# Performance work log

Measured on AMD Instinct MI355X. Metric: run time of the kernel, lower is better.

## Reference

```python
import jax, jax.numpy as jnp
import numpy as np

HIDDEN = 4096
NUM_Q = 32
NUM_KV = 8
HEAD_DIM = 128
EPS = 1e-6
ROPE_THETA = 1e6


def _rmsnorm(x, w):
    # x: [..., HEAD_DIM]
    var = jnp.mean(x * x, axis=-1, keepdims=True)
    return x * jax.lax.rsqrt(var + EPS) * w


def _rope(x, positions):
    # x: [n_tok, H, HEAD_DIM], rotate-half convention
    half = HEAD_DIM // 2
    inv_freq = 1.0 / (ROPE_THETA ** (jnp.arange(0, half, dtype=jnp.float32) / half))
    freqs = positions.astype(jnp.float32)[:, None] * inv_freq  # [n_tok, half]
    cos = jnp.concatenate([jnp.cos(freqs), jnp.cos(freqs)], axis=-1)[:, None, :]
    sin = jnp.concatenate([jnp.sin(freqs), jnp.sin(freqs)], axis=-1)[:, None, :]
    x1, x2 = x[..., :half], x[..., half:]
    rot = jnp.concatenate([-x2, x1], axis=-1)
    return x * cos + rot * sin


def setup_inputs() -> dict:
    key = jax.random.key(0)
    ks = jax.random.split(key, 7)
    n_tok = 2048
    s = 0.02
    return {
        "hidden": jax.random.normal(ks[0], (n_tok, HIDDEN), dtype=jnp.float32),
        "positions": jnp.arange(n_tok, dtype=jnp.int32),
        "Wq": jax.random.normal(ks[1], (HIDDEN, NUM_Q * HEAD_DIM), dtype=jnp.float32) * s,
        "Wk": jax.random.normal(ks[2], (HIDDEN, NUM_KV * HEAD_DIM), dtype=jnp.float32) * s,
        "Wv": jax.random.normal(ks[3], (HIDDEN, NUM_KV * HEAD_DIM), dtype=jnp.float32) * s,
        "Wo": jax.random.normal(ks[4], (NUM_Q * HEAD_DIM, HIDDEN), dtype=jnp.float32) * s,
        "q_norm_w": jnp.ones((HEAD_DIM,), dtype=jnp.float32),
        "k_norm_w": jnp.ones((HEAD_DIM,), dtype=jnp.float32),
    }


def reference(hidden, positions, Wq, Wk, Wv, Wo, q_norm_w, k_norm_w):
    n_tok = hidden.shape[0]
    group = NUM_Q // NUM_KV

    q = (hidden @ Wq).reshape(n_tok, NUM_Q, HEAD_DIM)
    k = (hidden @ Wk).reshape(n_tok, NUM_KV, HEAD_DIM)
    v = (hidden @ Wv).reshape(n_tok, NUM_KV, HEAD_DIM)

    q = _rmsnorm(q, q_norm_w)
    k = _rmsnorm(k, k_norm_w)
    q = _rope(q, positions)
    k = _rope(k, positions)

    # GQA: group q heads [n_tok, NUM_KV, group, HEAD_DIM]
    qg = q.reshape(n_tok, NUM_KV, group, HEAD_DIM)
    scale = 1.0 / np.sqrt(HEAD_DIM)
    scores = jnp.einsum("qhgd,khd->hgqk", qg, k) * scale  # [NUM_KV, group, n_tok, n_tok]
    causal = jnp.tril(jnp.ones((n_tok, n_tok), dtype=bool))
    scores = jnp.where(causal, scores, jnp.finfo(scores.dtype).min)
    probs = jax.nn.softmax(scores, axis=-1)
    out = jnp.einsum("hgqk,khd->qhgd", probs, v)  # [n_tok, NUM_KV, group, HEAD_DIM]
    out = out.reshape(n_tok, NUM_Q * HEAD_DIM)
    return out @ Wo
```

## Files before the change

kernel.cpp:

```cpp
#include <hip/hip_runtime.h>
#include <stdint.h>

typedef unsigned short u16;
typedef __bf16 bf16_t;
typedef bf16_t bf16x8 __attribute__((ext_vector_type(8)));
typedef float f32x4 __attribute__((ext_vector_type(4)));
typedef u16 u16x4 __attribute__((ext_vector_type(4)));
typedef u16 u16x8 __attribute__((ext_vector_type(8)));

#define HIDDEN 4096
#define NTOK 2048
#define NQ 32
#define NKV 8
#define HD 128
#define QKV_N 6144

__device__ __forceinline__ u16 f2bf(float f) {
  union { float f; uint32_t u; } v; v.f = f;
  uint32_t u = v.u;
  return (u16)((u + 0x7fffu + ((u >> 16) & 1u)) >> 16);
}

__global__ void cvt_hidden(const float* __restrict__ src, u16* __restrict__ dst, int n4) {
  int i = blockIdx.x * blockDim.x + threadIdx.x;
  if (i >= n4) return;
  float4 v = ((const float4*)src)[i];
  u16x4 o;
  o[0] = f2bf(v.x); o[1] = f2bf(v.y); o[2] = f2bf(v.z); o[3] = f2bf(v.w);
  ((u16x4*)dst)[i] = o;
}

__global__ void transpose_cvt(const float* __restrict__ src, u16* __restrict__ dst,
                              int R, int C) {
  __shared__ float tile[64][65];
  int tx = threadIdx.x & 63;
  int ty = threadIdx.x >> 6;
  int r0 = blockIdx.y * 64, c0 = blockIdx.x * 64;
  for (int i = 0; i < 16; i++) {
    int r = ty + i * 4;
    tile[r][tx] = src[(size_t)(r0 + r) * C + c0 + tx];
  }
  __syncthreads();
  for (int i = 0; i < 16; i++) {
    int c = ty + i * 4;
    dst[(size_t)(c0 + c) * R + r0 + tx] = f2bf(tile[tx][c]);
  }
}

__global__ __launch_bounds__(256) void gemm_bt(const u16* __restrict__ A,
                                               const u16* __restrict__ B,
                                               float* __restrict__ C,
                                               int M, int N, int K) {
  __shared__ u16 sA[128 * 32];
  __shared__ u16 sB[128 * 32];
  const int tid = threadIdx.x;
  const int wave = tid >> 6, lane = tid & 63;
  const int quad = lane >> 4, l16 = lane & 15;
  const int wy = wave >> 1, wx = wave & 1;
  const int row0 = blockIdx.y * 128, col0 = blockIdx.x * 128;
  f32x4 acc[4][4] = {};
  const int srow = wave * 32 + (lane >> 2);
  const int sk = (lane & 3) * 8;
  const u16* gA = A + (size_t)(row0 + srow) * K + sk;
  const u16* gB = B + (size_t)(col0 + srow) * K + sk;
  u16* lA = sA + wave * 32 * 32;
  u16* lB = sB + wave * 32 * 32;
  for (int k0 = 0; k0 < K; k0 += 32) {
    __builtin_amdgcn_global_load_lds(
        (__attribute__((address_space(1))) void*)(void*)(gA + k0),
        (__attribute__((address_space(3))) void*)(void*)lA, 16, 0, 0);
    __builtin_amdgcn_global_load_lds(
        (__attribute__((address_space(1))) void*)(void*)(gA + k0 + (size_t)16 * K),
        (__attribute__((address_space(3))) void*)(void*)(lA + 16 * 32), 16, 0, 0);
    __builtin_amdgcn_global_load_lds(
        (__attribute__((address_space(1))) void*)(void*)(gB + k0),
        (__attribute__((address_space(3))) void*)(void*)lB, 16, 0, 0);
    __builtin_amdgcn_global_load_lds(
        (__attribute__((address_space(1))) void*)(void*)(gB + k0 + (size_t)16 * K),
        (__attribute__((address_space(3))) void*)(void*)(lB + 16 * 32), 16, 0, 0);
    __syncthreads();
    bf16x8 af[4], bfr[4];
    for (int mi = 0; mi < 4; mi++)
      af[mi] = *(const bf16x8*)(const void*)(sA + (wy * 64 + mi * 16 + l16) * 32 + quad * 8);
    for (int ni = 0; ni < 4; ni++)
      bfr[ni] = *(const bf16x8*)(const void*)(sB + (wx * 64 + ni * 16 + l16) * 32 + quad * 8);
    for (int mi = 0; mi < 4; mi++)
      for (int ni = 0; ni < 4; ni++)
        acc[mi][ni] = __builtin_amdgcn_mfma_f32_16x16x32_bf16(af[mi], bfr[ni], acc[mi][ni], 0, 0, 0);
    __syncthreads();
  }
  for (int mi = 0; mi < 4; mi++)
    for (int ni = 0; ni < 4; ni++) {
      int row = row0 + wy * 64 + mi * 16 + quad * 4;
      int col = col0 + wx * 64 + ni * 16 + l16;
      float* cp = C + (size_t)row * N + col;
      for (int r = 0; r < 4; r++) cp[(size_t)r * N] = acc[mi][ni][r];
    }
}

__global__ void normrope(const float* __restrict__ qkv, const int* __restrict__ pos,
                         const float* __restrict__ qw, const float* __restrict__ kw,
                         u16* __restrict__ Qo, u16* __restrict__ Ko) {
  const int hh = blockIdx.x;
  const int t = blockIdx.y;
  const int lane = threadIdx.x;
  const bool isQ = hh < NQ;
  const int col = isQ ? hh * HD : HIDDEN + (hh - NQ) * HD;
  const float* src = qkv + (size_t)t * QKV_N + col;
  float x1 = src[lane], x2 = src[lane + 64];
  float ss = x1 * x1 + x2 * x2;
  for (int m = 1; m < 64; m <<= 1) ss += __shfl_xor(ss, m);
  float inv = rsqrtf(ss * (1.0f / 128.0f) + 1e-6f);
  const float* w = isQ ? qw : kw;
  x1 *= inv * w[lane];
  x2 *= inv * w[lane + 64];
  float p = (float)pos[t];
  float freq = expf((float)lane * -0.2158673525f);
  float a = p * freq;
  float sn = sinf(a), cs = cosf(a);
  float o1 = x1 * cs - x2 * sn;
  float o2 = x2 * cs + x1 * sn;
  const float osc = isQ ? 0.08838834764831845f : 1.0f;
  u16* dst = isQ ? (Qo + (size_t)t * (NQ * HD) + hh * HD)
                 : (Ko + (size_t)t * (NKV * HD) + (hh - NQ) * HD);
  dst[lane] = f2bf(o1 * osc);
  dst[lane + 64] = f2bf(o2 * osc);
}

__global__ void vtrans(const float* __restrict__ qkv, u16* __restrict__ vT) {
  __shared__ float s[128][65];
  int tb = blockIdx.x;
  int vh = blockIdx.y;
  int tid = threadIdx.x;
  for (int i = 0; i < 32; i++) {
    int e = i * 256 + tid;
    int tl = e >> 7;
    int d = e & 127;
    s[d][tl] = qkv[(size_t)(tb * 64 + tl) * QKV_N + 5120 + vh * 128 + d];
  }
  __syncthreads();
  for (int i = 0; i < 32; i++) {
    int e = i * 256 + tid;
    int d = e >> 6;
    int tl = e & 63;
    vT[(size_t)vh * (HD * NTOK) + (size_t)d * NTOK + tb * 64 + tl] = f2bf(s[d][tl]);
  }
}

__global__ __launch_bounds__(512) void flash2(const u16* __restrict__ Q,
                                              const u16* __restrict__ K,
                                              const u16* __restrict__ V,
                                              u16* __restrict__ O) {
  __shared__ u16 sK[64 * 136];
  __shared__ u16 sV[128 * 72];
  __shared__ u16 sP[8][16 * 72];
  const int p = blockIdx.x, h = blockIdx.y, kvh = h >> 2;
  const int tid = threadIdx.x;
  const int wave = tid >> 6, lane = tid & 63;
  const int quad = lane >> 4, l16 = lane & 15;
  u16* myP = &sP[wave][0];
  const u16* Vh = V + (size_t)kvh * (HD * NTOK);
  const int qtiles[2] = {p, 15 - p};
  const int rk0 = tid >> 4, ck0 = tid & 15;
  const int rv0 = tid >> 3, cv0 = tid & 7;
  for (int ti = 0; ti < 2; ti++) {
    const int qb = qtiles[ti];
    const int qrow0 = qb * 128 + wave * 16;
    bf16x8 qf[4];
    for (int ks = 0; ks < 4; ks++)
      qf[ks] = *(const bf16x8*)(const void*)(Q + (size_t)(qrow0 + l16) * (NQ * HD) + h * HD + ks * 32 + quad * 8);
    f32x4 accO[8] = {};
    float l_r[4] = {0.f, 0.f, 0.f, 0.f};
    const int nU = 2 * (qb + 1);
    const int myMax = (qrow0 + 15) >> 6;
    for (int kb = 0; kb < nU; kb++) {
      u16x8 k0 = *(const u16x8*)(const void*)(K + (size_t)(kb * 64 + rk0) * (NKV * HD) + kvh * HD + ck0 * 8);
      u16x8 k1 = *(const u16x8*)(const void*)(K + (size_t)(kb * 64 + rk0 + 32) * (NKV * HD) + kvh * HD + ck0 * 8);
      u16x8 v0 = *(const u16x8*)(const void*)(Vh + (size_t)rv0 * NTOK + kb * 64 + cv0 * 8);
      u16x8 v1 = *(const u16x8*)(const void*)(Vh + (size_t)(rv0 + 64) * NTOK + kb * 64 + cv0 * 8);
      __syncthreads();
      *(u16x8*)(void*)(sK + rk0 * 136 + ck0 * 8) = k0;
      *(u16x8*)(void*)(sK + (rk0 + 32) * 136 + ck0 * 8) = k1;
      *(u16x8*)(void*)(sV + rv0 * 72 + cv0 * 8) = v0;
      *(u16x8*)(void*)(sV + (rv0 + 64) * 72 + cv0 * 8) = v1;
      __syncthreads();
      if (kb <= myMax) {
        f32x4 s[4] = {};
        for (int ks = 0; ks < 4; ks++)
          for (int nt = 0; nt < 4; nt++) {
            bf16x8 kf = *(const bf16x8*)(const void*)(sK + (nt * 16 + l16) * 136 + ks * 32 + quad * 8);
            s[nt] = __builtin_amdgcn_mfma_f32_16x16x32_bf16(qf[ks], kf, s[nt], 0, 0, 0);
          }
        const int qg = qrow0 + quad * 4;
        for (int nt = 0; nt < 4; nt++) {
          int tok = kb * 64 + nt * 16 + l16;
          for (int r = 0; r < 4; r++) {
            float e = __expf(s[nt][r]);
            float pv = (tok <= qg + r) ? e : 0.0f;
            l_r[r] += pv;
            myP[(quad * 4 + r) * 72 + nt * 16 + l16] = f2bf(pv);
          }
        }
        asm volatile("s_waitcnt lgkmcnt(0)" ::: "memory");
        for (int ks = 0; ks < 2; ks++) {
          bf16x8 pf = *(const bf16x8*)(const void*)(myP + l16 * 72 + ks * 32 + quad * 8);
          for (int nt = 0; nt < 8; nt++) {
            bf16x8 vf = *(const bf16x8*)(const void*)(sV + (nt * 16 + l16) * 72 + ks * 32 + quad * 8);
            accO[nt] = __builtin_amdgcn_mfma_f32_16x16x32_bf16(pf, vf, accO[nt], 0, 0, 0);
          }
        }
      }
    }
    float inv[4];
    for (int r = 0; r < 4; r++) {
      float t = l_r[r];
      t += __shfl_xor(t, 1);
      t += __shfl_xor(t, 2);
      t += __shfl_xor(t, 4);
      t += __shfl_xor(t, 8);
      inv[r] = 1.0f / t;
    }
    for (int nt = 0; nt < 8; nt++)
      for (int r = 0; r < 4; r++)
        O[(size_t)(qrow0 + quad * 4 + r) * (NQ * HD) + h * HD + nt * 16 + l16] =
            f2bf(accO[nt][r] * inv[r]);
  }
}

extern "C" void kernel_launch(void* const* d_in, const int* in_sizes, int n_in,
                              void* d_out, int out_size, void* d_ws, size_t ws_size,
                              hipStream_t stream) {
  const float* hidden = (const float*)d_in[0];
  const int* positions = (const int*)d_in[1];
  const float* Wq = (const float*)d_in[2];
  const float* Wk = (const float*)d_in[3];
  const float* Wv = (const float*)d_in[4];
  const float* Wo = (const float*)d_in[5];
  const float* qw = (const float*)d_in[6];
  const float* kw = (const float*)d_in[7];
  char* ws = (char*)d_ws;
  u16* hid_bf  = (u16*)(ws);
  u16* WqkvT   = (u16*)(ws + 16777216);
  u16* WoT     = (u16*)(ws + 67108864);
  float* qkvf  = (float*)(ws + 100663296);
  u16* Qn      = (u16*)(ws + 150994944);
  u16* Kn      = (u16*)(ws + 167772160);
  u16* Vt      = (u16*)(ws + 171966464);
  u16* AO      = (u16*)(ws + 176160768);
  float* outp  = (float*)d_out;

  cvt_hidden<<<NTOK * HIDDEN / 4 / 256, 256, 0, stream>>>(hidden, hid_bf, NTOK * HIDDEN / 4);
  transpose_cvt<<<dim3(64, 64), 256, 0, stream>>>(Wq, WqkvT, 4096, 4096);
  transpose_cvt<<<dim3(16, 64), 256, 0, stream>>>(Wk, WqkvT + (size_t)4096 * 4096, 4096, 1024);
  transpose_cvt<<<dim3(16, 64), 256, 0, stream>>>(Wv, WqkvT + (size_t)5120 * 4096, 4096, 1024);
  transpose_cvt<<<dim3(64, 64), 256, 0, stream>>>(Wo, WoT, 4096, 4096);
  gemm_bt<<<dim3(48, 16), 256, 0, stream>>>(hid_bf, WqkvT, qkvf, 2048, 6144, 4096);
  normrope<<<dim3(40, 2048), 64, 0, stream>>>(qkvf, positions, qw, kw, Qn, Kn);
  vtrans<<<dim3(32, 8), 256, 0, stream>>>(qkvf, Vt);
  flash2<<<dim3(8, 32), 512, 0, stream>>>(Qn, Kn, Vt, AO);
  gemm_bt<<<dim3(32, 16), 256, 0, stream>>>(AO, WoT, outp, 2048, 4096, 4096);
}
```

Measured before the change: 567.1 us.

## Double GEMM K-tile to 64 with XOR-swizzled LDS and batch normrope tokens

The GEMM now stages a 64-wide K slice per iteration instead of 32, which halves the number of barriers per K. It XOR-swizzles the LDS column chunks so the 16-byte fragment reads avoid bank conflicts, and sets launch bounds to request 3 blocks per CU. The normrope kernel now handles four tokens per 256-thread block instead of one token per 64-thread block, which cuts block count and launch overhead. The larger LDS footprint (32KB per block) and doubled fragment registers may reduce occupancy.

Result: faster. 502.3 us (-11.4%).

```diff
diff --git a/kernel.cpp b/kernel.cpp
--- a/kernel.cpp
+++ b/kernel.cpp
@@ -14,6 +14,9 @@
 #define NKV 8
 #define HD 128
 #define QKV_N 6144
+
+#define AS1 __attribute__((address_space(1)))
+#define AS3 __attribute__((address_space(3)))
 
 __device__ __forceinline__ u16 f2bf(float f) {
   union { float f; uint32_t u; } v; v.f = f;
@@ -47,46 +50,46 @@
   }
 }
 
-__global__ __launch_bounds__(256) void gemm_bt(const u16* __restrict__ A,
-                                               const u16* __restrict__ B,
-                                               float* __restrict__ C,
-                                               int M, int N, int K) {
-  __shared__ u16 sA[128 * 32];
-  __shared__ u16 sB[128 * 32];
+__global__ __launch_bounds__(256, 3) void gemm_bt(const u16* __restrict__ A,
+                                                  const u16* __restrict__ B,
+                                                  float* __restrict__ C,
+                                                  int M, int N, int K) {
+  __shared__ u16 sA[128 * 64];
+  __shared__ u16 sB[128 * 64];
   const int tid = threadIdx.x;
   const int wave = tid >> 6, lane = tid & 63;
   const int quad = lane >> 4, l16 = lane & 15;
   const int wy = wave >> 1, wx = wave & 1;
   const int row0 = blockIdx.y * 128, col0 = blockIdx.x * 128;
   f32x4 acc[4][4] = {};
-  const int srow = wave * 32 + (lane >> 2);
-  const int sk = (lane & 3) * 8;
-  const u16* gA = A + (size_t)(row0 + srow) * K + sk;
-  const u16* gB = B + (size_t)(col0 + srow) * K + sk;
-  u16* lA = sA + wave * 32 * 32;
-  u16* lB = sB + wave * 32 * 32;
-  for (int k0 = 0; k0 < K; k0 += 32) {
-    __builtin_amdgcn_global_load_lds(
-        (__attribute__((address_space(1))) void*)(void*)(gA + k0),
-        (__attribute__((address_space(3))) void*)(void*)lA, 16, 0, 0);
-    __builtin_amdgcn_global_load_lds(
-        (__attribute__((address_space(1))) void*)(void*)(gA + k0 + (size_t)16 * K),
-        (__attribute__((address_space(3))) void*)(void*)(lA + 16 * 32), 16, 0, 0);
-    __builtin_amdgcn_global_load_lds(
-        (__attribute__((address_space(1))) void*)(void*)(gB + k0),
-        (__attribute__((address_space(3))) void*)(void*)lB, 16, 0, 0);
-    __builtin_amdgcn_global_load_lds(
-        (__attribute__((address_space(1))) void*)(void*)(gB + k0 + (size_t)16 * K),
-        (__attribute__((address_space(3))) void*)(void*)(lB + 16 * 32), 16, 0, 0);
+  const int lr = lane >> 3;
+  const int sc = (lane & 7) ^ lr;
+  const u16* gA = A + (size_t)(row0 + wave * 32 + lr) * K + sc * 8;
+  const u16* gB = B + (size_t)(col0 + wave * 32 + lr) * K + sc * 8;
+  u16* lA = sA + wave * 32 * 64;
+  u16* lB = sB + wave * 32 * 64;
+  const int swz = l16 & 7;
+  for (int k0 = 0; k0 < K; k0 += 64) {
+    for (int j = 0; j < 4; j++) {
+      __builtin_amdgcn_global_load_lds(
+          (AS1 void*)(void*)(gA + k0 + (size_t)(j * 8) * K),
+          (AS3 void*)(void*)(lA + j * 8 * 64), 16, 0, 0);
+      __builtin_amdgcn_global_load_lds(
+          (AS1 void*)(void*)(gB + k0 + (size_t)(j * 8) * K),
+          (AS3 void*)(void*)(lB + j * 8 * 64), 16, 0, 0);
+    }
     __syncthreads();
-    bf16x8 af[4], bfr[4];
-    for (int mi = 0; mi < 4; mi++)
-      af[mi] = *(const bf16x8*)(const void*)(sA + (wy * 64 + mi * 16 + l16) * 32 + quad * 8);
-    for (int ni = 0; ni < 4; ni++)
-      bfr[ni] = *(const bf16x8*)(const void*)(sB + (wx * 64 + ni * 16 + l16) * 32 + quad * 8);
-    for (int mi = 0; mi < 4; mi++)
-      for (int ni = 0; ni < 4; ni++)
-        acc[mi][ni] = __builtin_amdgcn_mfma_f32_16x16x32_bf16(af[mi], bfr[ni], acc[mi][ni], 0, 0, 0);
+    bf16x8 af[2][4], bfr[2][4];
+    for (int s = 0; s < 2; s++)
+      for (int mi = 0; mi < 4; mi++) {
+        const int c = ((s * 4 + quad) ^ swz) * 8;
+        af[s][mi] = *(const bf16x8*)(const void*)(sA + (wy * 64 + mi * 16 + l16) * 64 + c);
+        bfr[s][mi] = *(const bf16x8*)(const void*)(sB + (wx * 64 + mi * 16 + l16) * 64 + c);
+      }
+    for (int s = 0; s < 2; s++)
+      for (int mi = 0; mi < 4; mi++)
+        for (int ni = 0; ni < 4; ni++)
+          acc[mi][ni] = __builtin_amdgcn_mfma_f32_16x16x32_bf16(af[s][mi], bfr[s][ni], acc[mi][ni], 0, 0, 0);
     __syncthreads();
   }
   for (int mi = 0; mi < 4; mi++)
@@ -102,8 +105,8 @@
                          const float* __restrict__ qw, const float* __restrict__ kw,
                          u16* __restrict__ Qo, u16* __restrict__ Ko) {
   const int hh = blockIdx.x;
-  const int t = blockIdx.y;
-  const int lane = threadIdx.x;
+  const int t = blockIdx.y * 4 + (threadIdx.x >> 6);
+  const int lane = threadIdx.x & 63;
   const bool isQ = hh < NQ;
   const int col = isQ ? hh * HD : HIDDEN + (hh - NQ) * HD;
   const float* src = qkv + (size_t)t * QKV_N + col;
@@ -255,7 +258,7 @@
   transpose_cvt<<<dim3(16, 64), 256, 0, stream>>>(Wv, WqkvT + (size_t)5120 * 4096, 4096, 1024);
   transpose_cvt<<<dim3(64, 64), 256, 0, stream>>>(Wo, WoT, 4096, 4096);
   gemm_bt<<<dim3(48, 16), 256, 0, stream>>>(hid_bf, WqkvT, qkvf, 2048, 6144, 4096);
-  normrope<<<dim3(40, 2048), 64, 0, stream>>>(qkvf, positions, qw, kw, Qn, Kn);
+  normrope<<<dim3(40, 512), 256, 0, stream>>>(qkvf, positions, qw, kw, Qn, Kn);
   vtrans<<<dim3(32, 8), 256, 0, stream>>>(qkvf, Vt);
   flash2<<<dim3(8, 32), 512, 0, stream>>>(Qn, Kn, Vt, AO);
   gemm_bt<<<dim3(32, 16), 256, 0, stream>>>(AO, WoT, outp, 2048, 4096, 4096);
```
